# Optimization experiments

Measured on AMD Instinct MI355X. Metric: run time of the kernel, lower is better.

## Reference

```python
import jax, jax.numpy as jnp
import numpy as np
from functools import partial

# ---- NASA Li-ion battery default parameters (Daigle model) ----
P = {}
P['qMobile'] = 7600.0
P['xnMax'] = 0.6; P['xnMin'] = 0.0
P['xpMax'] = 1.0; P['xpMin'] = 0.4
P['qmax'] = P['qMobile'] / (P['xnMax'] - P['xnMin'])  # 12666.667
P['Ro'] = 0.117215
P['R'] = 8.3144621
P['F'] = 96487.0
P['alpha'] = 0.5
P['Sn'] = 0.000437545
P['Sp'] = 0.00030962
P['kn'] = 2120.96
P['kp'] = 248898.0
P['Volume'] = 2e-5
P['VolumeSurf'] = 0.1
P['tDiffusion'] = 7e6
P['to'] = 6.08671
P['tsn'] = 1001.38
P['tsp'] = 46.4311
P['VolS'] = P['VolumeSurf'] * P['Volume']
P['VolB'] = P['Volume'] - P['VolS']
P['qSMax'] = P['qmax'] * P['VolS'] / P['Volume']
P['qBMax'] = P['qmax'] * P['VolB'] / P['Volume']
U0P, U0N = 4.03, 0.01
APS = np.array([-31593.7, 0.106747, 24606.4, -78561.9, 13317.9, 307387.0,
                84916.1, -1.07469e6, 2285.04, 990894.0, 283920.0, -161513.0,
                -469218.0], dtype=np.float32)
ANS = np.array([86.19], dtype=np.float32)
DT = 1.0
B, T = 2048, 1024


def _vint(x, As, F):
    N = As.shape[0]
    k = jnp.arange(N, dtype=x.dtype)          # [N]
    ki = jnp.arange(N)
    b = (2.0 * x - 1.0)[..., None]            # [B,1]
    ab, sg = jnp.abs(b), jnp.sign(b)
    # integer-exponent pow with correct sign for negative base
    p_kp1 = ab ** (k + 1.0) * jnp.where((ki + 1) % 2 == 1, sg, 1.0)
    p_km1 = ab ** (k - 1.0) * jnp.where((ki - 1) % 2 != 0, sg, 1.0)
    term = p_kp1 - (2.0 * x * (1.0 - x))[..., None] * k * p_km1
    return (term @ As) / F


def _vint_safe(x, As, F):
    ok = x != 0.5
    sx = jnp.where(ok, x, 1.0)
    return jnp.where(ok, _vint(sx, As, F), 0.0)


def _step(state, i, Aps, Ans):
    tb, Vo, Vsn, Vsp, qnB, qnS, qpB, qpS = state
    R, F, alpha = P['R'], P['F'], P['alpha']
    xpS = qpS / P['qSMax']
    xnS = qnS / P['qSMax']
    Jn0 = P['kn'] * (1.0 - xnS) ** alpha * xnS ** alpha
    Jp0 = P['kp'] * (1.0 - xpS) ** alpha * xpS ** alpha
    dBSn = (qnB / P['VolB'] - qnS / P['VolS']) / P['tDiffusion']
    dBSp = (qpB / P['VolB'] - qpS / P['VolS']) / P['tDiffusion']
    Jn, Jp = i / P['Sn'], i / P['Sp']
    VoN = i * P['Ro']
    VsnN = R * tb / (F * alpha) * jnp.arcsinh(Jn / (2.0 * Jn0))
    VspN = R * tb / (F * alpha) * jnp.arcsinh(Jp / (2.0 * Jp0))
    Ven = U0N + R * tb / F * jnp.log((1.0 - xnS) / xnS) + _vint_safe(xnS, Ans, F)
    Vep = U0P + R * tb / F * jnp.log((1.0 - xpS) / xpS) + _vint_safe(xpS, Aps, F)
    v = Vep - Ven - Vo - Vsn - Vsp
    new = (tb,
           Vo + DT * (VoN - Vo) / P['to'],
           Vsn + DT * (VsnN - Vsn) / P['tsn'],
           Vsp + DT * (VspN - Vsp) / P['tsp'],
           qnB - DT * dBSn,
           qnS + DT * (dBSn - i),
           qpB - DT * dBSp,
           qpS + DT * (i + dBSp))
    return new, v


def setup_inputs() -> dict:
    key = jax.random.key(0)
    k1, = jax.random.split(key, 1)
    i = 0.1 + 0.9 * jax.random.uniform(k1, (B, T), dtype=jnp.float32)  # amps
    qnS0 = P['xnMax'] * P['qmax'] * P['VolS'] / P['Volume']
    qnB0 = P['xnMax'] * P['qmax'] * P['VolB'] / P['Volume']
    qpS0 = P['xpMin'] * P['qmax'] * P['VolS'] / P['Volume']
    qpB0 = P['xpMin'] * P['qmax'] * P['VolB'] / P['Volume']
    x0 = jnp.tile(jnp.array([292.1, 0.0, 0.0, 0.0, qnB0, qnS0, qpB0, qpS0],
                            dtype=jnp.float32), (B, 1))
    return {'i': i, 'x0': x0, 'Aps': jnp.asarray(APS), 'Ans': jnp.asarray(ANS)}


def reference(i, x0, Aps, Ans):
    state0 = tuple(x0[:, j] for j in range(8))
    def body(st, it):
        return _step(st, it, Aps, Ans)
    _, v = jax.lax.scan(body, state0, i.T)  # v: [T,B]
    return v.T  # voltage per cell per step, [B,T]
```

## Files before the change

kernel.cpp:

```cpp
#include <hip/hip_runtime.h>
#include <math.h>


constexpr int NTHR = 128;
constexpr int L = 8;

__global__ __launch_bounds__(NTHR, 4) void battery_scan3(
    const float* __restrict__ I, const float* __restrict__ X0,
    const float* __restrict__ Aps, const float* __restrict__ Ans,
    float* __restrict__ out, int Tn)
{
    const int cell = blockIdx.x;
    const int tid  = threadIdx.x;
    const int lane = tid & 63;
    const int wv   = tid >> 6;

    __shared__ float shA[3][2];
    __shared__ float shC[2][2];

    const float ivB    = (float)(1.0/1.8e-5);
    const float ivS    = (float)(1.0/2.0e-6);
    const float aq     = (float)(1.0 - (1.0/1.8e-5 + 1.0/2.0e-6)/7.0e6);
    const float ao     = (float)(1.0 - 1.0/6.08671);
    const float asn    = (float)(1.0 - 1.0/1001.38);
    const float asp    = (float)(1.0 - 1.0/46.4311);
    const float invSum = (float)(1.0/(1.0/1.8e-5 + 1.0/2.0e-6));
    const float cX     = (float)((1.0/(1.0/1.8e-5 + 1.0/2.0e-6)) / 1266.6666666666667);
    const float invF   = (float)(1.0/96487.0);
    const float c_zn   = (float)(0.5/0.000437545/2120.96);
    const float c_zp   = (float)(0.5/0.00030962/248898.0);
    const float Ro_to  = (float)(0.117215/6.08671);
    const float U0PN   = 4.03f - 0.01f;

    float aqp = 1.f, aop = 1.f, asnp = 1.f, aspp = 1.f;
    #pragma unroll
    for (int k = 0; k < L; ++k) { aqp *= aq; aop *= ao; asnp *= asn; aspp *= asp; }
    const float aqL = aqp, aoL = aop, asnL = asnp, aspL = aspp;

    const float tb   = X0[cell*8+0];
    const float Vo0  = X0[cell*8+1];
    const float Vsn0 = X0[cell*8+2];
    const float Vsp0 = X0[cell*8+3];
    const float qnB0 = X0[cell*8+4];
    const float qnS0 = X0[cell*8+5];
    const float qpB0 = X0[cell*8+6];
    const float qpS0 = X0[cell*8+7];
    const float An0F = Ans[0] * invF;

    const float rtf   = 8.3144621f * tb * invF;
    const float rtfa  = 2.f*rtf;
    const float bn_c  = rtfa * (float)(1.0/1001.38);
    const float bp_c  = rtfa * (float)(1.0/46.4311);
    const float u_n0  = qnB0 + qnS0;
    const float u_p0  = qpB0 + qpS0;
    const float w_n0  = qnB0*ivB - qnS0*ivS;
    const float w_p0  = qpB0*ivB - qpS0*ivS;

    const float fl = (float)lane;
    const float plq = exp2f(fl * __log2f(aqL));
    const float plo = exp2f(fl * __log2f(aoL));
    const float pln = exp2f(fl * __log2f(asnL));
    const float plp = exp2f(fl * __log2f(aspL));

    const float* ibase = I + (size_t)cell*Tn + tid*L;
    const float4 iva = *(const float4*)(ibase);
    const float4 ivb = *(const float4*)(ibase + 4);
    const float i8[8] = {iva.x, iva.y, iva.z, iva.w, ivb.x, ivb.y, ivb.z, ivb.w};

    auto wscan = [&](float tot, float RL, float& ep, float& Tw, float& R64) {
        float v = tot, r = RL;
        #pragma unroll
        for (int s = 1; s < 64; s <<= 1) {
            float p = __shfl_up(v, s);
            v = (lane >= s) ? fmaf(r, p, v) : v;
            r *= r;
        }
        float e = __shfl_up(v, 1);
        ep = (lane == 0) ? 0.f : e;
        Tw = __shfl(v, 63);
        R64 = r;
    };

    float ts = 0.f, tg = 0.f, to_ = 0.f;
    #pragma unroll
    for (int k = 0; k < L; ++k) {
        float b = i8[k];
        ts += b; tg = fmaf(aq, tg, b); to_ = fmaf(ao, to_, b);
    }
    float epS, TwS, RS, epG, TwG, RG, epO, TwO, RO;
    wscan(ts,  1.f, epS, TwS, RS);
    wscan(tg,  aqL, epG, TwG, RG);
    wscan(to_, aoL, epO, TwO, RO);
    if (lane == 0) { shA[0][wv] = TwS; shA[1][wv] = TwG; shA[2][wv] = TwO; }
    __syncthreads();
    float cs = epS, cg = epG, co = epO;
    float pwq = plq, pwo = plo;
    if (wv) {
        cs += shA[0][0];
        cg = fmaf(plq, shA[1][0], cg);
        co = fmaf(plo, shA[2][0], co);
        pwq *= RG; pwo *= RO;
    }

    float vpart[L], bsn[L], bsp[L];
    float S = cs, G = cg, O = co;
    float hwn = pwq*w_n0, hwp = pwq*w_p0;
    float hvo = pwo*Vo0;
    float rn = 0.f, rp = 0.f;
    #pragma unroll
    for (int k = 0; k < L; ++k) {
        float it  = i8[k];
        float u_n = u_n0 - S, u_p = u_p0 + S;
        float w_n = fmaf( ivS, G, hwn);
        float w_p = fmaf(-ivS, G, hwp);
        float xnS = (fmaf(u_n, ivB, -w_n)) * cX;
        float xpS = (fmaf(u_p, ivB, -w_p)) * cX;
        float Vo_t = fmaf(Ro_to, O, hvo);
        S += it; G = fmaf(aq, G, it); O = fmaf(ao, O, it);
        hwn *= aq; hwp *= aq; hvo *= ao;

        float pn = fmaf(-xnS, xnS, xnS);
        float pp = fmaf(-xpS, xpS, xpS);
        float zn = it * c_zn * rsqrtf(pn);
        float zp = it * c_zp * rsqrtf(pp);
        float asn_n = __logf(zn + sqrtf(fmaf(zn, zn, 1.f)));
        float zp2  = zp*zp;
        float asn_p = zp * fmaf(-0.16666667f, zp2, 1.f);
        bsn[k] = bn_c * asn_n;
        bsp[k] = bp_c * asn_p;
        rn = fmaf(asn, rn, bsn[k]);
        rp = fmaf(asp, rp, bsp[k]);

        float omxn = 1.f - xnS, omxp = 1.f - xpS;
        float lr = __logf(__fdividef(omxp * xnS, xpS * omxn));

        float b_ = fmaf(2.f, xpS, -1.f);
        float P = 0.f, D = 0.f;
        #pragma unroll
        for (int j = 12; j >= 0; --j) {
            D = fmaf(D, b_, P);
            P = fmaf(P, b_, Aps[j]);
        }
        float pp2 = pp + pp;
        float vint_p = (b_*P - pp2*D) * invF;
        vint_p = (xpS != 0.5f) ? vint_p : 0.f;
        float vint_n = An0F * fmaf(2.f, xnS, -1.f);

        vpart[k] = U0PN + fmaf(rtf, lr, vint_p - vint_n - Vo_t);
    }

    float epN, TwN, RN, epP, TwP, RP;
    wscan(rn, asnL, epN, TwN, RN);
    wscan(rp, aspL, epP, TwP, RP);
    if (lane == 0) { shC[0][wv] = TwN; shC[1][wv] = TwP; }
    __syncthreads();
    float csn = epN, csp = epP;
    float pwn = pln, pwp = plp;
    if (wv) {
        csn = fmaf(pln, shC[0][0], csn);
        csp = fmaf(plp, shC[1][0], csp);
        pwn *= RN; pwp *= RP;
    }

    float N = csn, Pv = csp;
    float hn = pwn*Vsn0, hp = pwp*Vsp0;
    #pragma unroll
    for (int k = 0; k < L; ++k) {
        vpart[k] -= (hn + N) + (hp + Pv);
        N  = fmaf(asn, N,  bsn[k]);
        Pv = fmaf(asp, Pv, bsp[k]);
        hn *= asn; hp *= asp;
    }

    float* obase = out + (size_t)cell*Tn + tid*L;
    *(float4*)(obase)     = make_float4(vpart[0], vpart[1], vpart[2], vpart[3]);
    *(float4*)(obase + 4) = make_float4(vpart[4], vpart[5], vpart[6], vpart[7]);
}

extern "C" void kernel_launch(void* const* d_in, const int* in_sizes, int n_in,
                              void* d_out, int out_size, void* d_ws, size_t ws_size,
                              hipStream_t stream) {
    const float* I   = (const float*)d_in[0];
    const float* X0  = (const float*)d_in[1];
    const float* Aps = (const float*)d_in[2];
    const float* Ans = (const float*)d_in[3];
    float* out = (float*)d_out;

    int Bn = in_sizes[1] / 8;
    int Tn = in_sizes[0] / Bn;

    battery_scan3<<<dim3(Bn), dim3(NTHR), 0, stream>>>(I, X0, Aps, Ans, out, Tn);
}
```

Measured before the change: 72.27 us.

## Precompute Redlich-Kister coefficients, truncate decayed scans, scalarize per-cell constants

Folds the positive-electrode Redlich-Kister expression into a single even/odd-split polynomial in (2x-1) with coefficients precomputed once per thread, replacing the value/derivative Horner loop and the x == 0.5 guard. The intra-wave scans for strongly decaying recurrences now run fewer shuffle steps, since contributions from distant lanes are treated as negligible. Per-cell constants are made wave-uniform with readfirstlane, compile-time constants replace runtime products, and the per-step state recurrences are merged into fewer multiply-adds. The truncated scans and the reworked polynomial change rounding slightly, which could affect numerical accuracy.

```diff
diff --git a/kernel.cpp b/kernel.cpp
--- a/kernel.cpp
+++ b/kernel.cpp
@@ -3,9 +3,39 @@
 
 
 constexpr int NTHR = 128;
-constexpr int L = 8;
-
-__global__ __launch_bounds__(NTHR, 4) void battery_scan3(
+constexpr int L    = 8;
+
+constexpr double d_ivB = 1.0/1.8e-5;
+constexpr double d_ivS = 1.0/2.0e-6;
+constexpr double d_aq  = 1.0 - (d_ivB + d_ivS)/7.0e6;
+constexpr double d_ao  = 1.0 - 1.0/6.08671;
+constexpr double d_asn = 1.0 - 1.0/1001.38;
+constexpr double d_asp = 1.0 - 1.0/46.4311;
+constexpr double d_qS  = 1266.6666666666667;
+constexpr double d_iSum= 1.0/(d_ivB + d_ivS);
+constexpr double d_cX  = d_iSum/d_qS;
+
+constexpr double dpow(double a, int n){ double r = 1.0; for (int i = 0; i < n; ++i) r *= a; return r; }
+
+__device__ __forceinline__ float rfl(float x){
+    return __int_as_float(__builtin_amdgcn_readfirstlane(__float_as_int(x)));
+}
+
+template<int STEPS>
+__device__ __forceinline__ void wscan(float tot, float RL, int lane, float& ep, float& Tw){
+    float v = tot, r = RL;
+    #pragma unroll
+    for (int s = 1; s < (1 << STEPS); s <<= 1){
+        float p = __shfl_up(v, s);
+        v = (lane >= s) ? fmaf(r, p, v) : v;
+        r *= r;
+    }
+    float e = __shfl_up(v, 1);
+    ep = (lane == 0) ? 0.f : e;
+    Tw = __shfl(v, 63);
+}
+
+__global__ __launch_bounds__(NTHR, 4) void battery_scan4(
     const float* __restrict__ I, const float* __restrict__ X0,
     const float* __restrict__ Aps, const float* __restrict__ Ans,
     float* __restrict__ out, int Tn)
@@ -18,24 +48,30 @@
     __shared__ float shA[3][2];
     __shared__ float shC[2][2];
 
-    const float ivB    = (float)(1.0/1.8e-5);
-    const float ivS    = (float)(1.0/2.0e-6);
-    const float aq     = (float)(1.0 - (1.0/1.8e-5 + 1.0/2.0e-6)/7.0e6);
-    const float ao     = (float)(1.0 - 1.0/6.08671);
-    const float asn    = (float)(1.0 - 1.0/1001.38);
-    const float asp    = (float)(1.0 - 1.0/46.4311);
-    const float invSum = (float)(1.0/(1.0/1.8e-5 + 1.0/2.0e-6));
-    const float cX     = (float)((1.0/(1.0/1.8e-5 + 1.0/2.0e-6)) / 1266.6666666666667);
-    const float invF   = (float)(1.0/96487.0);
-    const float c_zn   = (float)(0.5/0.000437545/2120.96);
-    const float c_zp   = (float)(0.5/0.00030962/248898.0);
-    const float Ro_to  = (float)(0.117215/6.08671);
-    const float U0PN   = 4.03f - 0.01f;
-
-    float aqp = 1.f, aop = 1.f, asnp = 1.f, aspp = 1.f;
-    #pragma unroll
-    for (int k = 0; k < L; ++k) { aqp *= aq; aop *= ao; asnp *= asn; aspp *= asp; }
-    const float aqL = aqp, aoL = aop, asnL = asnp, aspL = aspp;
+    constexpr float aq    = (float)d_aq;
+    constexpr float ao    = (float)d_ao;
+    constexpr float asn   = (float)d_asn;
+    constexpr float asp   = (float)d_asp;
+    constexpr float aqL   = (float)dpow(d_aq,  L);
+    constexpr float aoL   = (float)dpow(d_ao,  L);
+    constexpr float asnL  = (float)dpow(d_asn, L);
+    constexpr float aspL  = (float)dpow(d_asp, L);
+    constexpr float RG64  = (float)dpow(d_aq,  64*L);
+    constexpr float RO64  = (float)dpow(d_ao,  64*L);
+    constexpr float RN64  = (float)dpow(d_asn, 64*L);
+    constexpr float RP64  = (float)dpow(d_asp, 64*L);
+    constexpr float kS    = (float)(d_ivB*d_cX);
+    constexpr float ivScX = (float)(d_ivS*d_cX);
+    constexpr float cXf   = (float)d_cX;
+    constexpr float ivB   = (float)d_ivB;
+    constexpr float ivS   = (float)d_ivS;
+    constexpr float invF  = (float)(1.0/96487.0);
+    constexpr float c_zn  = (float)(0.5/(0.000437545*2120.96));
+    constexpr float c_zp  = (float)(0.5/(0.00030962*248898.0));
+    constexpr float Ro_to = (float)(0.117215/6.08671);
+    constexpr float cBn   = (float)(2.0/1001.38);
+    constexpr float cBp   = (float)(2.0/46.4311);
+    constexpr float U0PN  = (float)(4.03 - 0.01);
 
     const float tb   = X0[cell*8+0];
     const float Vo0  = X0[cell*8+1];
@@ -45,18 +81,25 @@
     const float qnS0 = X0[cell*8+5];
     const float qpB0 = X0[cell*8+6];
     const float qpS0 = X0[cell*8+7];
-    const float An0F = Ans[0] * invF;
-
-    const float rtf   = 8.3144621f * tb * invF;
-    const float rtfa  = 2.f*rtf;
-    const float bn_c  = rtfa * (float)(1.0/1001.38);
-    const float bp_c  = rtfa * (float)(1.0/46.4311);
-    const float u_n0  = qnB0 + qnS0;
-    const float u_p0  = qpB0 + qpS0;
-    const float w_n0  = qnB0*ivB - qnS0*ivS;
-    const float w_p0  = qpB0*ivB - qpS0*ivS;
-
-    const float fl = (float)lane;
+
+    const float rtf  = rfl(8.3144621f * tb * invF);
+    const float bn_c = rfl(rtf * cBn);
+    const float bp_c = rfl(rtf * cBp);
+    const float An0F = rfl(Ans[0] * invF);
+    const float k0n  = rfl((qnB0 + qnS0) * kS);
+    const float k0p  = rfl((qpB0 + qpS0) * kS);
+    const float wn0c = rfl(fmaf(qnB0, ivB, -qnS0*ivS) * cXf);
+    const float wp0c = rfl(fmaf(qpB0, ivB, -qpS0*ivS) * cXf);
+
+    float c_[14];
+    #pragma unroll
+    for (int j = 0; j < 14; ++j){
+        float am1 = (j >= 1)  ? Aps[j-1] : 0.f;
+        float ap1 = (j <= 11) ? Aps[j+1] : 0.f;
+        c_[j] = rfl(0.5f * (float)(j+1) * (am1 - ap1));
+    }
+
+    const float fl  = (float)lane;
     const float plq = exp2f(fl * __log2f(aqL));
     const float plo = exp2f(fl * __log2f(aoL));
     const float pln = exp2f(fl * __log2f(asnL));
@@ -67,109 +110,101 @@
     const float4 ivb = *(const float4*)(ibase + 4);
     const float i8[8] = {iva.x, iva.y, iva.z, iva.w, ivb.x, ivb.y, ivb.z, ivb.w};
 
-    auto wscan = [&](float tot, float RL, float& ep, float& Tw, float& R64) {
-        float v = tot, r = RL;
-        #pragma unroll
-        for (int s = 1; s < 64; s <<= 1) {
-            float p = __shfl_up(v, s);
-            v = (lane >= s) ? fmaf(r, p, v) : v;
-            r *= r;
-        }
-        float e = __shfl_up(v, 1);
-        ep = (lane == 0) ? 0.f : e;
-        Tw = __shfl(v, 63);
-        R64 = r;
-    };
-
     float ts = 0.f, tg = 0.f, to_ = 0.f;
     #pragma unroll
-    for (int k = 0; k < L; ++k) {
+    for (int k = 0; k < L; ++k){
         float b = i8[k];
         ts += b; tg = fmaf(aq, tg, b); to_ = fmaf(ao, to_, b);
     }
-    float epS, TwS, RS, epG, TwG, RG, epO, TwO, RO;
-    wscan(ts,  1.f, epS, TwS, RS);
-    wscan(tg,  aqL, epG, TwG, RG);
-    wscan(to_, aoL, epO, TwO, RO);
-    if (lane == 0) { shA[0][wv] = TwS; shA[1][wv] = TwG; shA[2][wv] = TwO; }
+    float epS, TwS, epG, TwG, epO, TwO;
+    wscan<6>(ts,  1.f, lane, epS, TwS);
+    wscan<4>(tg,  aqL, lane, epG, TwG);
+    wscan<3>(to_, aoL, lane, epO, TwO);
+    if (lane == 0){ shA[0][wv] = TwS; shA[1][wv] = TwG; shA[2][wv] = TwO; }
     __syncthreads();
     float cs = epS, cg = epG, co = epO;
     float pwq = plq, pwo = plo;
-    if (wv) {
+    if (wv){
         cs += shA[0][0];
-        cg = fmaf(plq, shA[1][0], cg);
-        co = fmaf(plo, shA[2][0], co);
-        pwq *= RG; pwo *= RO;
-    }
-
+        cg  = fmaf(plq, shA[1][0], cg);
+        co  = fmaf(plo, shA[2][0], co);
+        pwq *= RG64; pwo *= RO64;
+    }
+
+    float S  = cs;
+    float Wn = fmaf( ivScX, cg, pwq * wn0c);
+    float Wp = fmaf(-ivScX, cg, pwq * wp0c);
+    float VO = fmaf( Ro_to, co, pwo * Vo0);
     float vpart[L], bsn[L], bsp[L];
-    float S = cs, G = cg, O = co;
-    float hwn = pwq*w_n0, hwp = pwq*w_p0;
-    float hvo = pwo*Vo0;
     float rn = 0.f, rp = 0.f;
     #pragma unroll
-    for (int k = 0; k < L; ++k) {
-        float it  = i8[k];
-        float u_n = u_n0 - S, u_p = u_p0 + S;
-        float w_n = fmaf( ivS, G, hwn);
-        float w_p = fmaf(-ivS, G, hwp);
-        float xnS = (fmaf(u_n, ivB, -w_n)) * cX;
-        float xpS = (fmaf(u_p, ivB, -w_p)) * cX;
-        float Vo_t = fmaf(Ro_to, O, hvo);
-        S += it; G = fmaf(aq, G, it); O = fmaf(ao, O, it);
-        hwn *= aq; hwp *= aq; hvo *= ao;
-
-        float pn = fmaf(-xnS, xnS, xnS);
-        float pp = fmaf(-xpS, xpS, xpS);
+    for (int k = 0; k < L; ++k){
+        const float it = i8[k];
+        float xn = fmaf(-kS, S, k0n) - Wn;
+        float xp = fmaf( kS, S, k0p) - Wp;
+        const float Vo_t = VO;
+        S += it;
+        float itc = it * ivScX;
+        Wn = fmaf(aq, Wn,  itc);
+        Wp = fmaf(aq, Wp, -itc);
+        VO = fmaf(ao, VO, it * Ro_to);
+
+        float pn = fmaf(-xn, xn, xn);
+        float pp = fmaf(-xp, xp, xp);
         float zn = it * c_zn * rsqrtf(pn);
         float zp = it * c_zp * rsqrtf(pp);
         float asn_n = __logf(zn + sqrtf(fmaf(zn, zn, 1.f)));
-        float zp2  = zp*zp;
+        float zp2   = zp * zp;
         float asn_p = zp * fmaf(-0.16666667f, zp2, 1.f);
         bsn[k] = bn_c * asn_n;
         bsp[k] = bp_c * asn_p;
         rn = fmaf(asn, rn, bsn[k]);
         rp = fmaf(asp, rp, bsp[k]);
 
-        float omxn = 1.f - xnS, omxp = 1.f - xpS;
-        float lr = __logf(__fdividef(omxp * xnS, xpS * omxn));
-
-        float b_ = fmaf(2.f, xpS, -1.f);
-        float P = 0.f, D = 0.f;
-        #pragma unroll
-        for (int j = 12; j >= 0; --j) {
-            D = fmaf(D, b_, P);
-            P = fmaf(P, b_, Aps[j]);
-        }
-        float pp2 = pp + pp;
-        float vint_p = (b_*P - pp2*D) * invF;
-        vint_p = (xpS != 0.5f) ? vint_p : 0.f;
-        float vint_n = An0F * fmaf(2.f, xnS, -1.f);
-
-        vpart[k] = U0PN + fmaf(rtf, lr, vint_p - vint_n - Vo_t);
-    }
-
-    float epN, TwN, RN, epP, TwP, RP;
-    wscan(rn, asnL, epN, TwN, RN);
-    wscan(rp, aspL, epP, TwP, RP);
-    if (lane == 0) { shC[0][wv] = TwN; shC[1][wv] = TwP; }
+        float omxn = 1.f - xn, omxp = 1.f - xp;
+        float lr = __logf(__fdividef(omxp * xn, xp * omxn));
+
+        float b_ = fmaf(2.f, xp, -1.f);
+        float t2 = b_ * b_;
+        float po = c_[13];
+        po = fmaf(po, t2, c_[11]);
+        po = fmaf(po, t2, c_[9]);
+        po = fmaf(po, t2, c_[7]);
+        po = fmaf(po, t2, c_[5]);
+        po = fmaf(po, t2, c_[3]);
+        po = fmaf(po, t2, c_[1]);
+        float pe = c_[12];
+        pe = fmaf(pe, t2, c_[10]);
+        pe = fmaf(pe, t2, c_[8]);
+        pe = fmaf(pe, t2, c_[6]);
+        pe = fmaf(pe, t2, c_[4]);
+        pe = fmaf(pe, t2, c_[2]);
+        pe = fmaf(pe, t2, c_[0]);
+        float vint_p = fmaf(b_, po, pe) * invF;
+        float vint_n = An0F * fmaf(2.f, xn, -1.f);
+
+        vpart[k] = fmaf(rtf, lr, (U0PN - Vo_t) + (vint_p - vint_n));
+    }
+
+    float epN, TwN, epP, TwP;
+    wscan<6>(rn, asnL, lane, epN, TwN);
+    wscan<5>(rp, aspL, lane, epP, TwP);
+    if (lane == 0){ shC[0][wv] = TwN; shC[1][wv] = TwP; }
     __syncthreads();
     float csn = epN, csp = epP;
     float pwn = pln, pwp = plp;
-    if (wv) {
+    if (wv){
         csn = fmaf(pln, shC[0][0], csn);
         csp = fmaf(plp, shC[1][0], csp);
-        pwn *= RN; pwp *= RP;
-    }
-
-    float N = csn, Pv = csp;
-    float hn = pwn*Vsn0, hp = pwp*Vsp0;
-    #pragma unroll
-    for (int k = 0; k < L; ++k) {
-        vpart[k] -= (hn + N) + (hp + Pv);
+        pwn *= RN64; pwp *= RP64;
+    }
+    float N  = fmaf(pwn, Vsn0, csn);
+    float Pv = fmaf(pwp, Vsp0, csp);
+    #pragma unroll
+    for (int k = 0; k < L; ++k){
+        vpart[k] -= (N + Pv);
         N  = fmaf(asn, N,  bsn[k]);
         Pv = fmaf(asp, Pv, bsp[k]);
-        hn *= asn; hp *= asp;
     }
 
     float* obase = out + (size_t)cell*Tn + tid*L;
@@ -189,5 +224,5 @@
     int Bn = in_sizes[1] / 8;
     int Tn = in_sizes[0] / Bn;
 
-    battery_scan3<<<dim3(Bn), dim3(NTHR), 0, stream>>>(I, X0, Aps, Ans, out, Tn);
-}
+    battery_scan4<<<dim3(Bn), dim3(NTHR), 0, stream>>>(I, X0, Aps, Ans, out, Tn);
+}
```

Measured after the change: 71.89 us. About the same (-0.5%).
